# Kernel tuning notes

Hardware: AMD Instinct MI355X
Metric: run time of the kernel (lower is better)

## Reference

```python
import jax, jax.numpy as jnp
import numpy as np

N_NODES = 50000
N_EDGES = 800000
NEG_SLOPE = 0.2  # GATConv default
BN_EPS = 1e-5


def _seg_softmax(logits, seg, n):
    # per-target-node softmax over incoming edges (PyG softmax w/ +1e-16)
    m = jax.ops.segment_max(logits, seg, num_segments=n)
    m = jnp.where(jnp.isfinite(m), m, 0.0)
    e = jnp.exp(logits - m[seg])
    s = jax.ops.segment_sum(e, seg, num_segments=n)
    return e / (s[seg] + 1e-16)


def _gat_conv(x, src, dst, W, a_src, a_dst, b, concat):
    # x: [N, Fin]; W: [Fin, H*C]; a_src/a_dst: [H, C]
    n = x.shape[0]
    H, C = a_src.shape
    h = (x @ W).reshape(n, H, C)
    al_s = jnp.einsum('nhc,hc->nh', h, a_src)
    al_d = jnp.einsum('nhc,hc->nh', h, a_dst)
    logits = jax.nn.leaky_relu(al_s[src] + al_d[dst], NEG_SLOPE)  # [E, H]
    alpha = _seg_softmax(logits, dst, n)                           # [E, H]
    out = jax.ops.segment_sum(h[src] * alpha[:, :, None], dst, num_segments=n)
    out = out.reshape(n, H * C) if concat else out.mean(axis=1)
    return out + b


def _bn(x, g, b):
    mu = jnp.mean(x, axis=0)
    var = jnp.mean((x - mu) ** 2, axis=0)
    return (x - mu) * jax.lax.rsqrt(var + BN_EPS) * g + b


def _gat_params(key, fin, heads, ch, scale=0.1):
    k1, k2, k3 = jax.random.split(key, 3)
    W = jax.random.normal(k1, (fin, heads * ch), jnp.float32) * scale
    a_s = jax.random.normal(k2, (heads, ch), jnp.float32) * scale
    a_d = jax.random.normal(k3, (heads, ch), jnp.float32) * scale
    return W, a_s, a_d


def setup_inputs() -> dict:
    key = jax.random.key(0)
    ks = jax.random.split(key, 12)
    inp = {}
    inp['x'] = jax.random.normal(ks[0], (N_NODES, 3), jnp.float32)
    inp['edge_index'] = jax.random.randint(ks[1], (2, N_EDGES), 0, N_NODES, jnp.int64 if jax.config.jax_enable_x64 else jnp.int32)
    inp['W11'], inp['as11'], inp['ad11'] = _gat_params(ks[2], 3, 8, 8)
    inp['b11'] = jnp.zeros((64,), jnp.float32)
    inp['W12'], inp['as12'], inp['ad12'] = _gat_params(ks[3], 64, 8, 8)
    inp['b12'] = jnp.zeros((64,), jnp.float32)
    inp['g1'] = jnp.ones((64,), jnp.float32)
    inp['be1'] = jnp.zeros((64,), jnp.float32)
    inp['W21'], inp['as21'], inp['ad21'] = _gat_params(ks[4], 64, 8, 32)
    inp['b21'] = jnp.zeros((256,), jnp.float32)
    inp['W22'], inp['as22'], inp['ad22'] = _gat_params(ks[5], 256, 8, 32)
    inp['b22'] = jnp.zeros((256,), jnp.float32)
    inp['g2'] = jnp.ones((256,), jnp.float32)
    inp['be2'] = jnp.zeros((256,), jnp.float32)
    inp['W31'], inp['as31'], inp['ad31'] = _gat_params(ks[6], 256, 8, 64)
    inp['b31'] = jnp.zeros((512,), jnp.float32)
    inp['W32'], inp['as32'], inp['ad32'] = _gat_params(ks[7], 512, 8, 1)
    inp['b32'] = jnp.zeros((1,), jnp.float32)
    return inp


def reference(x, edge_index,
              W11, as11, ad11, b11, W12, as12, ad12, b12, g1, be1,
              W21, as21, ad21, b21, W22, as22, ad22, b22, g2, be2,
              W31, as31, ad31, b31, W32, as32, ad32, b32):
    n = x.shape[0]
    loops = jnp.arange(n, dtype=edge_index.dtype)
    src = jnp.concatenate([edge_index[0], loops])  # add_self_loops=True
    dst = jnp.concatenate([edge_index[1], loops])
    # GAT(3, 64, 2): conv -> relu -> conv
    h = jax.nn.relu(_gat_conv(x, src, dst, W11, as11, ad11, b11, True))
    h = _gat_conv(h, src, dst, W12, as12, ad12, b12, True)
    h = jax.nn.leaky_relu(_bn(h, g1, be1), 0.1)
    # GAT(64, 256, 2)
    h = jax.nn.relu(_gat_conv(h, src, dst, W21, as21, ad21, b21, True))
    h = _gat_conv(h, src, dst, W22, as22, ad22, b22, True)
    h = jax.nn.leaky_relu(_bn(h, g2, be2), 0.1)
    # GAT(256, 512, 2, 1): conv -> relu -> conv(concat=False)
    h = jax.nn.relu(_gat_conv(h, src, dst, W31, as31, ad31, b31, True))
    h = _gat_conv(h, src, dst, W32, as32, ad32, b32, False)
    return jax.nn.sigmoid(h)
```

## Files before the change

### kernel.cpp

```cpp
#include <hip/hip_runtime.h>
#include <math.h>

typedef short short8 __attribute__((ext_vector_type(8)));
typedef short short4v __attribute__((ext_vector_type(4)));
typedef float f32x4 __attribute__((ext_vector_type(4)));

__device__ __forceinline__ unsigned short f2bf(float v){
  unsigned u = __builtin_bit_cast(unsigned, v);
  u += 0x7FFFu + ((u >> 16) & 1u);
  return (unsigned short)(u >> 16);
}
__device__ __forceinline__ float bf2f(unsigned short b){
  unsigned u = ((unsigned)b) << 16;
  return __builtin_bit_cast(float, u);
}

__global__ void k_deg(const int* __restrict__ dstv, int* __restrict__ deg, int E){
  int e = blockIdx.x*blockDim.x + threadIdx.x;
  if (e < E) atomicAdd(&deg[dstv[e]], 1);
}

__global__ void k_scan(const int* __restrict__ deg, int* __restrict__ off,
                       int* __restrict__ cursor, int N){
  __shared__ int sh[1024];
  __shared__ int carry_s;
  int t = threadIdx.x;
  if (t == 0) carry_s = 0;
  __syncthreads();
  for (int base = 0; base < N; base += 1024){
    int i = base + t;
    int v = (i < N) ? deg[i] : 0;
    sh[t] = v;
    __syncthreads();
    for (int d = 1; d < 1024; d <<= 1){
      int tmp = (t >= d) ? sh[t-d] : 0;
      __syncthreads();
      sh[t] += tmp;
      __syncthreads();
    }
    int inc = sh[t];
    int c = carry_s;
    if (i < N){ off[i+1] = c + inc; cursor[i] = c + inc - v; }
    __syncthreads();
    if (t == 1023) carry_s = c + sh[1023];
    __syncthreads();
  }
  if (t == 0) off[0] = 0;
}

__global__ void k_fill(const int* __restrict__ srcv, const int* __restrict__ dstv,
                       int* __restrict__ cursor, int* __restrict__ csr, int E){
  int e = blockIdx.x*blockDim.x + threadIdx.x;
  if (e < E){
    int d = dstv[e];
    int p = atomicAdd(&cursor[d], 1);
    csr[p] = srcv[e];
  }
}

__global__ void k_prepB(const float* __restrict__ W, unsigned short* __restrict__ bh,
                        unsigned short* __restrict__ bl, int K, int kpshift, int Nn){
  int Kp = 1 << kpshift;
  int i = blockIdx.x*blockDim.x + threadIdx.x;
  if (i >= Nn*Kp) return;
  int n = i >> kpshift, k = i & (Kp-1);
  float v = (k < K) ? W[(size_t)k*Nn + n] : 0.0f;
  unsigned short h = f2bf(v);
  bh[i] = h;
  bl[i] = f2bf(v - bf2f(h));
}

template<int BN>
__global__ __launch_bounds__((BN==64)?256:512)
void gemm_mfma(const float* __restrict__ A, const unsigned short* __restrict__ Bh,
               const unsigned short* __restrict__ Bl,
               const float* __restrict__ a_s, const float* __restrict__ a_d,
               unsigned short* __restrict__ Pb, float* __restrict__ D, int M, int K){
  constexpr int WAVES   = (BN==64) ? 4 : 8;
  constexpr int BLOCK   = WAVES*64;
  constexpr int WAVES_N = BN/64;
  constexpr int WAVES_M = WAVES/WAVES_N;
  constexpr int WM      = 64/WAVES_M;
  constexpr int MF      = WM/16;
  constexpr int CH      = (BN==512)?64 : (BN==256)?32 : 8;
  const int Kp = (K + 63) & ~(int)63;

  __shared__ char lds[16384];

  int tid  = threadIdx.x;
  int lane = tid & 63;
  int wid  = tid >> 6;
  int wn = wid % WAVES_N;
  int wm = wid / WAVES_N;
  int n0w = wn*64;
  int wm0 = wm*WM;
  int m0 = blockIdx.x * 64;

  f32x4 acc[MF][4];
  #pragma unroll
  for (int i = 0; i < MF; ++i)
    #pragma unroll
    for (int j = 0; j < 4; ++j)
      acc[i][j] = (f32x4){0.f,0.f,0.f,0.f};

  constexpr int SITER = 512/BLOCK;

  for (int k0 = 0; k0 < Kp; k0 += 64){
    __syncthreads();
    #pragma unroll
    for (int it = 0; it < SITER; ++it){
      int i = it*BLOCK + tid;
      int row = i >> 3, c8 = i & 7;
      int gm = m0 + row;
      int gk = k0 + c8*8;
      float v[8];
      if (gm < M && gk + 8 <= K){
        const float* ap = A + (size_t)gm*K + gk;
        float4 x0 = *(const float4*)ap;
        float4 x1 = *(const float4*)(ap+4);
        v[0]=x0.x; v[1]=x0.y; v[2]=x0.z; v[3]=x0.w;
        v[4]=x1.x; v[5]=x1.y; v[6]=x1.z; v[7]=x1.w;
      } else {
        #pragma unroll
        for (int j=0;j<8;++j){
          int gkj = gk + j;
          v[j] = (gm < M && gkj < K) ? A[(size_t)gm*K + gkj] : 0.0f;
        }
      }
      short8 hi, lo;
      #pragma unroll
      for (int j=0;j<8;++j){
        unsigned short hb = f2bf(v[j]);
        hi[j] = (short)hb;
        lo[j] = (short)f2bf(v[j] - bf2f(hb));
      }
      int off = row*128 + ((c8 ^ (row&7))<<4);
      *(short8*)(lds + off) = hi;
      *(short8*)(lds + 8192 + off) = lo;
    }
    __syncthreads();
    #pragma unroll
    for (int kk = 0; kk < 2; ++kk){
      short8 bhf[4], blf[4];
      #pragma unroll
      for (int nf = 0; nf < 4; ++nf){
        int ncol = n0w + nf*16 + (lane & 15);
        int kidx = k0 + kk*32 + ((lane>>4)<<3);
        size_t bo = (size_t)ncol*Kp + kidx;
        bhf[nf] = *(const short8*)(Bh + bo);
        blf[nf] = *(const short8*)(Bl + bo);
      }
      #pragma unroll
      for (int mt = 0; mt < MF; ++mt){
        int row = wm0 + mt*16 + (lane & 15);
        int c8 = kk*4 + (lane>>4);
        int off = row*128 + ((c8 ^ (row&7))<<4);
        short8 ah = *(const short8*)(lds + off);
        short8 al = *(const short8*)(lds + 8192 + off);
        #pragma unroll
        for (int nf = 0; nf < 4; ++nf){
          acc[mt][nf] = __builtin_amdgcn_mfma_f32_16x16x32_bf16(ah, bhf[nf], acc[mt][nf], 0,0,0);
          acc[mt][nf] = __builtin_amdgcn_mfma_f32_16x16x32_bf16(ah, blf[nf], acc[mt][nf], 0,0,0);
          acc[mt][nf] = __builtin_amdgcn_mfma_f32_16x16x32_bf16(al, bhf[nf], acc[mt][nf], 0,0,0);
        }
      }
    }
  }

  float asv[4], adv[4];
  #pragma unroll
  for (int nf=0; nf<4; ++nf){
    int gcol = n0w + nf*16 + (lane&15);
    asv[nf] = a_s[gcol];
    adv[nf] = a_d[gcol];
  }
  #pragma unroll
  for (int mt = 0; mt < MF; ++mt){
    #pragma unroll
    for (int r = 0; r < 4; ++r){
      int gm = m0 + wm0 + mt*16 + ((lane>>4)<<2) + r;
      bool ok = gm < M;
      #pragma unroll
      for (int nf=0;nf<4;++nf){
        if (ok) Pb[(size_t)gm*BN + n0w + nf*16 + (lane&15)] = f2bf(acc[mt][nf][r]);
      }
      float* dp = D + (size_t)gm*16;
      if constexpr (CH == 64){
        float ps = acc[mt][0][r]*asv[0] + acc[mt][1][r]*asv[1]
                 + acc[mt][2][r]*asv[2] + acc[mt][3][r]*asv[3];
        float pd = acc[mt][0][r]*adv[0] + acc[mt][1][r]*adv[1]
                 + acc[mt][2][r]*adv[2] + acc[mt][3][r]*adv[3];
        #pragma unroll
        for (int d2=1; d2<16; d2<<=1){ ps += __shfl_xor(ps,d2,64); pd += __shfl_xor(pd,d2,64); }
        if (ok && (lane&15)==0){
          int head = n0w >> 6;
          dp[head] = ps;
          dp[8 + head] = pd;
        }
      } else if constexpr (CH == 32){
        float ps0 = acc[mt][0][r]*asv[0] + acc[mt][1][r]*asv[1];
        float ps1 = acc[mt][2][r]*asv[2] + acc[mt][3][r]*asv[3];
        float pd0 = acc[mt][0][r]*adv[0] + acc[mt][1][r]*adv[1];
        float pd1 = acc[mt][2][r]*adv[2] + acc[mt][3][r]*adv[3];
        #pragma unroll
        for (int d2=1; d2<16; d2<<=1){
          ps0 += __shfl_xor(ps0,d2,64); ps1 += __shfl_xor(ps1,d2,64);
          pd0 += __shfl_xor(pd0,d2,64); pd1 += __shfl_xor(pd1,d2,64);
        }
        if (ok && (lane&15)==0){
          int head = n0w >> 5;
          dp[head]     = ps0;
          dp[head + 1] = ps1;
          dp[8 + head]     = pd0;
          dp[8 + head + 1] = pd1;
        }
      } else {
        #pragma unroll
        for (int nf=0;nf<4;++nf){
          float ps = acc[mt][nf][r]*asv[nf];
          float pd = acc[mt][nf][r]*adv[nf];
          #pragma unroll
          for (int d2=1; d2<8; d2<<=1){ ps += __shfl_xor(ps,d2,64); pd += __shfl_xor(pd,d2,64); }
          if (ok && (lane&7)==0){
            int head = nf*2 + ((lane>>3)&1);
            dp[head]     = ps;
            dp[8 + head] = pd;
          }
        }
      }
    }
  }
}

__global__ __launch_bounds__(256)
void gemm_f32(const float* __restrict__ A, const float* __restrict__ B,
              float* __restrict__ C, int M, int K, int Nn){
  __shared__ float As[16][65];
  __shared__ float Bs[16][64];
  int tid = threadIdx.x;
  int tx = tid & 15, ty = tid >> 4;
  int m0 = blockIdx.x * 64, n0 = blockIdx.y * 64;
  float acc[4][4] = {};
  for (int k0 = 0; k0 < K; k0 += 16){
    #pragma unroll
    for (int it = 0; it < 4; ++it){
      int idx = it*256 + tid;
      int mm = idx >> 4, kk = idx & 15;
      int gm = m0 + mm, gk = k0 + kk;
      As[kk][mm] = (gm < M && gk < K) ? A[(size_t)gm*K + gk] : 0.0f;
    }
    #pragma unroll
    for (int it = 0; it < 4; ++it){
      int idx = it*256 + tid;
      int kk = idx >> 6, nn = idx & 63;
      int gk = k0 + kk, gn = n0 + nn;
      Bs[kk][nn] = (gk < K && gn < Nn) ? B[(size_t)gk*Nn + gn] : 0.0f;
    }
    __syncthreads();
    #pragma unroll
    for (int kk = 0; kk < 16; ++kk){
      float a[4], b[4];
      #pragma unroll
      for (int i = 0; i < 4; ++i) a[i] = As[kk][ty*4+i];
      #pragma unroll
      for (int j = 0; j < 4; ++j) b[j] = Bs[kk][tx*4+j];
      #pragma unroll
      for (int i = 0; i < 4; ++i)
        #pragma unroll
        for (int j = 0; j < 4; ++j)
          acc[i][j] += a[i]*b[j];
    }
    __syncthreads();
  }
  #pragma unroll
  for (int i = 0; i < 4; ++i){
    int gm = m0 + ty*4 + i;
    if (gm >= M) continue;
    int gn = n0 + tx*4;
    #pragma unroll
    for (int j = 0; j < 4; ++j)
      if (gn + j < Nn) C[(size_t)gm*Nn + gn + j] = acc[i][j];
  }
}

__global__ void k_attn8(const float* __restrict__ ht, const float* __restrict__ a_s,
                        const float* __restrict__ a_d, float* __restrict__ als,
                        float* __restrict__ ald, int N){
  int i = blockIdx.x*blockDim.x + threadIdx.x;
  if (i >= N*8) return;
  int h = i & 7;
  float v = ht[i];
  als[i] = v * a_s[h];
  ald[i] = v * a_d[h];
}

template<int HC, int ACT>
__global__ __launch_bounds__(256)
void k_agg(const unsigned short* __restrict__ Pb, const float* __restrict__ D,
           const int* __restrict__ off, const int* __restrict__ csr,
           const float* __restrict__ bias, float* __restrict__ outb, int N){
  constexpr int R = HC/64;
  __shared__ float salpha[4][512];
  int lane = threadIdx.x & 63;
  int wid  = threadIdx.x >> 6;
  int n = blockIdx.x*4 + wid;
  if (n >= N) return;
  int o0 = off[n], deg = off[n+1]-o0;
  int myh = lane >> 3;

  float aldn[8];
  {
    const float* dn = D + (size_t)n*16 + 8;
    float4 x0 = *(const float4*)dn;
    float4 x1 = *(const float4*)(dn+4);
    aldn[0]=x0.x; aldn[1]=x0.y; aldn[2]=x0.z; aldn[3]=x0.w;
    aldn[4]=x1.x; aldn[5]=x1.y; aldn[6]=x1.z; aldn[7]=x1.w;
  }

  float acc[R];
  #pragma unroll
  for (int j=0;j<R;++j) acc[j]=0.f;

  if (deg < 64){
    int nE = deg + 1;
    int myidx = (lane < deg) ? csr[o0+lane] : n;
    bool active = (lane < nE);
    float v[8];
    {
      const float* dp = D + (size_t)myidx*16;
      float4 x0 = *(const float4*)dp;
      float4 x1 = *(const float4*)(dp+4);
      float t[8] = {x0.x,x0.y,x0.z,x0.w,x1.x,x1.y,x1.z,x1.w};
      #pragma unroll
      for (int h=0;h<8;++h){
        float u = t[h] + aldn[h];
        u = u > 0.f ? u : 0.2f*u;
        v[h] = active ? u : -1e30f;
      }
    }
    float m[8];
    #pragma unroll
    for (int h=0;h<8;++h) m[h]=v[h];
    #pragma unroll
    for (int d=1; d<64; d<<=1)
      #pragma unroll
      for (int h=0;h<8;++h) m[h] = fmaxf(m[h], __shfl_xor(m[h], d, 64));
    float sv[8], s[8];
    #pragma unroll
    for (int h=0;h<8;++h){ sv[h] = active ? __expf(v[h]-m[h]) : 0.f; s[h]=sv[h]; }
    #pragma unroll
    for (int d=1; d<64; d<<=1)
      #pragma unroll
      for (int h=0;h<8;++h) s[h] += __shfl_xor(s[h], d, 64);
    if (active){
      #pragma unroll
      for (int h=0;h<8;++h) salpha[wid][lane*8+h] = sv[h] / (s[h] + 1e-16f);
    }
    asm volatile("s_waitcnt lgkmcnt(0)" ::: "memory");

    for (int e=0; e<nE; ++e){
      int src = __shfl(myidx, e, 64);
      float alpha = salpha[wid][e*8 + myh];
      const unsigned short* hp = Pb + (size_t)src*HC + lane*R;
      if constexpr (R == 1){
        acc[0] += alpha * bf2f(hp[0]);
      } else if constexpr (R == 4){
        short4v w = *(const short4v*)hp;
        #pragma unroll
        for (int j=0;j<4;++j) acc[j] += alpha * bf2f((unsigned short)w[j]);
      } else {
        short8 w = *(const short8*)hp;
        #pragma unroll
        for (int j=0;j<8;++j) acc[j] += alpha * bf2f((unsigned short)w[j]);
      }
    }
  } else {
    float m[8];
    #pragma unroll
    for (int h=0;h<8;++h) m[h] = -1e30f;
    for (int e = lane; e <= deg; e += 64){
      int src = (e < deg) ? csr[o0+e] : n;
      const float* ap = D + (size_t)src*16;
      #pragma unroll
      for (int h=0;h<8;++h){
        float u = ap[h] + aldn[h];
        u = u > 0.f ? u : 0.2f*u;
        m[h] = fmaxf(m[h], u);
      }
    }
    #pragma unroll
    for (int d=1; d<64; d<<=1)
      #pragma unroll
      for (int h=0;h<8;++h) m[h] = fmaxf(m[h], __shfl_xor(m[h], d, 64));
    float s[8] = {0,0,0,0,0,0,0,0};
    for (int e = lane; e <= deg; e += 64){
      int src = (e < deg) ? csr[o0+e] : n;
      const float* ap = D + (size_t)src*16;
      #pragma unroll
      for (int h=0;h<8;++h){
        float u = ap[h] + aldn[h];
        u = u > 0.f ? u : 0.2f*u;
        s[h] += __expf(u - m[h]);
      }
    }
    #pragma unroll
    for (int d=1; d<64; d<<=1)
      #pragma unroll
      for (int h=0;h<8;++h) s[h] += __shfl_xor(s[h], d, 64);
    float mh = m[myh];
    float rsh = 1.0f/(s[myh] + 1e-16f);
    float adh = aldn[myh];
    for (int e = 0; e <= deg; ++e){
      int src = (e < deg) ? csr[o0+e] : n;
      float u = D[(size_t)src*16 + myh] + adh;
      u = u > 0.f ? u : 0.2f*u;
      float alpha = __expf(u - mh) * rsh;
      const unsigned short* hp = Pb + (size_t)src*HC + lane*R;
      if constexpr (R == 1){
        acc[0] += alpha * bf2f(hp[0]);
      } else if constexpr (R == 4){
        short4v w = *(const short4v*)hp;
        #pragma unroll
        for (int j=0;j<4;++j) acc[j] += alpha * bf2f((unsigned short)w[j]);
      } else {
        short8 w = *(const short8*)hp;
        #pragma unroll
        for (int j=0;j<8;++j) acc[j] += alpha * bf2f((unsigned short)w[j]);
      }
    }
  }

  #pragma unroll
  for (int j = 0; j < R; ++j){
    int f = lane*R + j;
    float v = acc[j] + bias[f];
    if (ACT == 1) v = fmaxf(v, 0.0f);
    outb[(size_t)n*HC + f] = v;
  }
}

__global__ void k_bn_stats(const float* __restrict__ x, float* __restrict__ gsum,
                           float* __restrict__ gsq, int N, int HC){
  int f = threadIdx.x;
  float s = 0.f, q = 0.f;
  for (int r = blockIdx.x; r < N; r += gridDim.x){
    float v = x[(size_t)r*HC + f];
    s += v; q += v*v;
  }
  atomicAdd(&gsum[f], s);
  atomicAdd(&gsq[f], q);
}

__global__ void k_bn_apply(float* __restrict__ x, const float* __restrict__ gsum,
                           const float* __restrict__ gsq, const float* __restrict__ g,
                           const float* __restrict__ b, int N, int HC){
  int i = blockIdx.x*blockDim.x + threadIdx.x;
  int total = N*HC;
  if (i >= total) return;
  int f = i % HC;
  float inv = 1.0f/(float)N;
  float mu  = gsum[f]*inv;
  float var = gsq[f]*inv - mu*mu;
  float v = (x[i]-mu)*rsqrtf(var+1e-5f)*g[f] + b[f];
  x[i] = v > 0.f ? v : 0.1f*v;
}

__global__ void k_final(const float* __restrict__ ht8, const float* __restrict__ als,
                        const float* __restrict__ ald, const int* __restrict__ off,
                        const int* __restrict__ csr, const float* __restrict__ b32,
                        float* __restrict__ outp, int N){
  int n = blockIdx.x*blockDim.x + threadIdx.x;
  if (n >= N) return;
  int o0 = off[n], deg = off[n+1]-o0;
  float aldn[8], m[8], s[8], agg[8];
  #pragma unroll
  for (int h = 0; h < 8; ++h){ aldn[h] = ald[n*8+h]; m[h] = -1e30f; s[h]=0.f; agg[h]=0.f; }
  for (int e = 0; e <= deg; ++e){
    int src = (e < deg) ? csr[o0+e] : n;
    #pragma unroll
    for (int h = 0; h < 8; ++h){
      float v = als[(size_t)src*8+h] + aldn[h];
      v = v > 0.f ? v : 0.2f*v;
      m[h] = fmaxf(m[h], v);
    }
  }
  for (int e = 0; e <= deg; ++e){
    int src = (e < deg) ? csr[o0+e] : n;
    #pragma unroll
    for (int h = 0; h < 8; ++h){
      float v = als[(size_t)src*8+h] + aldn[h];
      v = v > 0.f ? v : 0.2f*v;
      float ex = __expf(v - m[h]);
      s[h] += ex;
      agg[h] += ex * ht8[(size_t)src*8+h];
    }
  }
  float o = 0.f;
  #pragma unroll
  for (int h = 0; h < 8; ++h) o += agg[h]/(s[h]+1e-16f);
  o = o*0.125f + b32[0];
  outp[n] = 1.0f/(1.0f + __expf(-o));
}

extern "C" void kernel_launch(void* const* d_in, const int* in_sizes, int n_in,
                              void* d_out, int out_size, void* d_ws, size_t ws_size,
                              hipStream_t stream){
  int N = in_sizes[0]/3;
  int E = in_sizes[1]/2;
  const float* x    = (const float*)d_in[0];
  const int*   ei   = (const int*)  d_in[1];
  const float* W11  = (const float*)d_in[2];
  const float* as11 = (const float*)d_in[3];
  const float* ad11 = (const float*)d_in[4];
  const float* b11  = (const float*)d_in[5];
  const float* W12  = (const float*)d_in[6];
  const float* as12 = (const float*)d_in[7];
  const float* ad12 = (const float*)d_in[8];
  const float* b12  = (const float*)d_in[9];
  const float* g1   = (const float*)d_in[10];
  const float* be1  = (const float*)d_in[11];
  const float* W21  = (const float*)d_in[12];
  const float* as21 = (const float*)d_in[13];
  const float* ad21 = (const float*)d_in[14];
  const float* b21  = (const float*)d_in[15];
  const float* W22  = (const float*)d_in[16];
  const float* as22 = (const float*)d_in[17];
  const float* ad22 = (const float*)d_in[18];
  const float* b22  = (const float*)d_in[19];
  const float* g2   = (const float*)d_in[20];
  const float* be2  = (const float*)d_in[21];
  const float* W31  = (const float*)d_in[22];
  const float* as31 = (const float*)d_in[23];
  const float* ad31 = (const float*)d_in[24];
  const float* b31  = (const float*)d_in[25];
  const float* W32  = (const float*)d_in[26];
  const float* as32 = (const float*)d_in[27];
  const float* ad32 = (const float*)d_in[28];
  const float* b32  = (const float*)d_in[29];

  char* ws = (char*)d_ws;
  size_t o = 0;
  auto alloc = [&](size_t bytes)->char*{
    char* p = ws + o;
    o = (o + bytes + 255) & ~(size_t)255;
    return p;
  };
  int*   deg    = (int*)  alloc((size_t)N*4);
  int*   off    = (int*)  alloc((size_t)(N+1)*4);
  int*   cursor = (int*)  alloc((size_t)N*4);
  int*   csr    = (int*)  alloc((size_t)E*4);
  unsigned short* bth = (unsigned short*)alloc(131072*2);
  unsigned short* btl = (unsigned short*)alloc(131072*2);
  float* als8   = (float*)alloc((size_t)N*8*4);
  float* ald8   = (float*)alloc((size_t)N*8*4);
  float* h8     = (float*)alloc((size_t)N*8*4);
  float* bsum   = (float*)alloc(256*4);
  float* bsq    = (float*)alloc(256*4);
  unsigned short* Pb = (unsigned short*)alloc((size_t)N*512*2);
  float* D      = (float*)alloc((size_t)N*16*4);
  float* Q      = (float*)alloc((size_t)N*512*4);
  (void)ws_size;

  hipMemsetAsync(deg, 0, (size_t)N*4, stream);
  int eb = (E+255)/256;
  k_deg <<<eb, 256, 0, stream>>>(ei+E, deg, E);
  k_scan<<<1, 1024, 0, stream>>>(deg, off, cursor, N);
  k_fill<<<eb, 256, 0, stream>>>(ei, ei+E, cursor, csr, E);

  int mb = (N+63)/64;
  int nb4 = (N+3)/4;

  k_prepB<<<(64*64)/256, 256, 0, stream>>>(W11, bth, btl, 3, 6, 64);
  gemm_mfma<64><<<mb, 256, 0, stream>>>(x, bth, btl, as11, ad11, Pb, D, N, 3);
  k_agg<64,1><<<nb4, 256, 0, stream>>>(Pb, D, off, csr, b11, Q, N);

  k_prepB<<<(64*64)/256, 256, 0, stream>>>(W12, bth, btl, 64, 6, 64);
  gemm_mfma<64><<<mb, 256, 0, stream>>>(Q, bth, btl, as12, ad12, Pb, D, N, 64);
  k_agg<64,0><<<nb4, 256, 0, stream>>>(Pb, D, off, csr, b12, Q, N);
  hipMemsetAsync(bsum, 0, 64*4, stream);
  hipMemsetAsync(bsq,  0, 64*4, stream);
  k_bn_stats<<<512, 64, 0, stream>>>(Q, bsum, bsq, N, 64);
  k_bn_apply<<<(N*64+255)/256, 256, 0, stream>>>(Q, bsum, bsq, g1, be1, N, 64);

  k_prepB<<<(256*64)/256, 256, 0, stream>>>(W21, bth, btl, 64, 6, 256);
  gemm_mfma<256><<<mb, 512, 0, stream>>>(Q, bth, btl, as21, ad21, Pb, D, N, 64);
  k_agg<256,1><<<nb4, 256, 0, stream>>>(Pb, D, off, csr, b21, Q, N);

  k_prepB<<<(256*256)/256, 256, 0, stream>>>(W22, bth, btl, 256, 8, 256);
  gemm_mfma<256><<<mb, 512, 0, stream>>>(Q, bth, btl, as22, ad22, Pb, D, N, 256);
  k_agg<256,0><<<nb4, 256, 0, stream>>>(Pb, D, off, csr, b22, Q, N);
  hipMemsetAsync(bsum, 0, 256*4, stream);
  hipMemsetAsync(bsq,  0, 256*4, stream);
  k_bn_stats<<<512, 256, 0, stream>>>(Q, bsum, bsq, N, 256);
  k_bn_apply<<<(N*256+255)/256, 256, 0, stream>>>(Q, bsum, bsq, g2, be2, N, 256);

  k_prepB<<<(512*256)/256, 256, 0, stream>>>(W31, bth, btl, 256, 8, 512);
  gemm_mfma<512><<<mb, 512, 0, stream>>>(Q, bth, btl, as31, ad31, Pb, D, N, 256);
  k_agg<512,1><<<nb4, 256, 0, stream>>>(Pb, D, off, csr, b31, Q, N);

  {
    dim3 g((N+63)/64, 1);
    gemm_f32<<<g, 256, 0, stream>>>(Q, W32, h8, N, 512, 8);
  }
  k_attn8<<<(N*8+255)/256, 256, 0, stream>>>(h8, as32, ad32, als8, ald8, N);
  k_final<<<(N+255)/256, 256, 0, stream>>>(h8, als8, ald8, off, csr, b32,
                                           (float*)d_out, N);
}
```

Before: 1.251 ms.

## Fuse BN into GEMM loads, wave-parallel final layer, shuffle-based scan

Several independent changes land together. The BatchNorm apply pass is replaced by a tiny coefficient kernel, and the scale/shift plus leaky-ReLU are folded into the GEMM's A-tile load, removing a full read/write pass over the activations. The last aggregation writes bf16, and a new wave-per-row dot-product kernel replaces the tiled fp32 GEMM for the 512->8 projection. The final softmax-aggregate kernel now uses one wave per node with shuffle reductions instead of one thread per node. The degree scan also switches to wave shuffles. Rounding the 512-wide input of the last projection to bf16 adds precision loss.

Result: faster. 1.146 ms (-8.4%).

```diff
diff --git a/kernel.cpp b/kernel.cpp
--- a/kernel.cpp
+++ b/kernel.cpp
@@ -22,30 +22,44 @@
 
 __global__ void k_scan(const int* __restrict__ deg, int* __restrict__ off,
                        int* __restrict__ cursor, int N){
-  __shared__ int sh[1024];
-  __shared__ int carry_s;
-  int t = threadIdx.x;
-  if (t == 0) carry_s = 0;
+  __shared__ int wpre[16];
+  __shared__ int s_tot;
+  __shared__ int carry;
+  int tid = threadIdx.x;
+  int lane = tid & 63, wv = tid >> 6;
+  if (tid == 0) carry = 0;
   __syncthreads();
   for (int base = 0; base < N; base += 1024){
-    int i = base + t;
+    int i = base + tid;
     int v = (i < N) ? deg[i] : 0;
-    sh[t] = v;
+    int incl = v;
+    #pragma unroll
+    for (int d = 1; d < 64; d <<= 1){
+      int t = __shfl_up(incl, d, 64);
+      if (lane >= d) incl += t;
+    }
+    if (lane == 63) wpre[wv] = incl;
     __syncthreads();
-    for (int d = 1; d < 1024; d <<= 1){
-      int tmp = (t >= d) ? sh[t-d] : 0;
-      __syncthreads();
-      sh[t] += tmp;
-      __syncthreads();
-    }
-    int inc = sh[t];
-    int c = carry_s;
-    if (i < N){ off[i+1] = c + inc; cursor[i] = c + inc - v; }
+    if (tid < 16){
+      int x = wpre[tid];
+      int ix = x;
+      #pragma unroll
+      for (int d = 1; d < 16; d <<= 1){
+        int t = __shfl_up(ix, d, 16);
+        if (tid >= d) ix += t;
+      }
+      wpre[tid] = ix - x;
+      if (tid == 15) s_tot = ix;
+    }
     __syncthreads();
-    if (t == 1023) carry_s = c + sh[1023];
+    int c = carry;
+    int excl = c + wpre[wv] + (incl - v);
+    if (i < N){ off[i+1] = excl + v; cursor[i] = excl; }
     __syncthreads();
-  }
-  if (t == 0) off[0] = 0;
+    if (tid == 0) carry = c + s_tot;
+    __syncthreads();
+  }
+  if (tid == 0) off[0] = 0;
 }
 
 __global__ void k_fill(const int* __restrict__ srcv, const int* __restrict__ dstv,
@@ -70,10 +84,24 @@
   bl[i] = f2bf(v - bf2f(h));
 }
 
-template<int BN>
+__global__ void k_bn_coef(const float* __restrict__ bsum, const float* __restrict__ bsq,
+                          const float* __restrict__ g, const float* __restrict__ b,
+                          float* __restrict__ sc, float* __restrict__ sh,
+                          float invN, int HC){
+  int f = threadIdx.x + blockIdx.x*blockDim.x;
+  if (f >= HC) return;
+  float mu  = bsum[f]*invN;
+  float var = bsq[f]*invN - mu*mu;
+  float rs  = rsqrtf(var + 1e-5f) * g[f];
+  sc[f] = rs;
+  sh[f] = b[f] - mu*rs;
+}
+
+template<int BN, int MODE>
 __global__ __launch_bounds__((BN==64)?256:512)
 void gemm_mfma(const float* __restrict__ A, const unsigned short* __restrict__ Bh,
                const unsigned short* __restrict__ Bl,
+               const float* __restrict__ bnsc, const float* __restrict__ bnsh,
                const float* __restrict__ a_s, const float* __restrict__ a_d,
                unsigned short* __restrict__ Pb, float* __restrict__ D, int M, int K){
   constexpr int WAVES   = (BN==64) ? 4 : 8;
@@ -120,11 +148,26 @@
         float4 x1 = *(const float4*)(ap+4);
         v[0]=x0.x; v[1]=x0.y; v[2]=x0.z; v[3]=x0.w;
         v[4]=x1.x; v[5]=x1.y; v[6]=x1.z; v[7]=x1.w;
+        if constexpr (MODE == 1){
+          #pragma unroll
+          for (int j=0;j<8;++j){
+            float u = v[j]*bnsc[gk+j] + bnsh[gk+j];
+            v[j] = u > 0.f ? u : 0.1f*u;
+          }
+        }
       } else {
         #pragma unroll
         for (int j=0;j<8;++j){
           int gkj = gk + j;
-          v[j] = (gm < M && gkj < K) ? A[(size_t)gm*K + gkj] : 0.0f;
+          bool ok = (gm < M && gkj < K);
+          float u = ok ? A[(size_t)gm*K + gkj] : 0.0f;
+          if constexpr (MODE == 1){
+            if (ok){
+              u = u*bnsc[gkj] + bnsh[gkj];
+              u = u > 0.f ? u : 0.1f*u;
+            }
+          }
+          v[j] = u;
         }
       }
       short8 hi, lo;
@@ -232,73 +275,11 @@
   }
 }
 
-__global__ __launch_bounds__(256)
-void gemm_f32(const float* __restrict__ A, const float* __restrict__ B,
-              float* __restrict__ C, int M, int K, int Nn){
-  __shared__ float As[16][65];
-  __shared__ float Bs[16][64];
-  int tid = threadIdx.x;
-  int tx = tid & 15, ty = tid >> 4;
-  int m0 = blockIdx.x * 64, n0 = blockIdx.y * 64;
-  float acc[4][4] = {};
-  for (int k0 = 0; k0 < K; k0 += 16){
-    #pragma unroll
-    for (int it = 0; it < 4; ++it){
-      int idx = it*256 + tid;
-      int mm = idx >> 4, kk = idx & 15;
-      int gm = m0 + mm, gk = k0 + kk;
-      As[kk][mm] = (gm < M && gk < K) ? A[(size_t)gm*K + gk] : 0.0f;
-    }
-    #pragma unroll
-    for (int it = 0; it < 4; ++it){
-      int idx = it*256 + tid;
-      int kk = idx >> 6, nn = idx & 63;
-      int gk = k0 + kk, gn = n0 + nn;
-      Bs[kk][nn] = (gk < K && gn < Nn) ? B[(size_t)gk*Nn + gn] : 0.0f;
-    }
-    __syncthreads();
-    #pragma unroll
-    for (int kk = 0; kk < 16; ++kk){
-      float a[4], b[4];
-      #pragma unroll
-      for (int i = 0; i < 4; ++i) a[i] = As[kk][ty*4+i];
-      #pragma unroll
-      for (int j = 0; j < 4; ++j) b[j] = Bs[kk][tx*4+j];
-      #pragma unroll
-      for (int i = 0; i < 4; ++i)
-        #pragma unroll
-        for (int j = 0; j < 4; ++j)
-          acc[i][j] += a[i]*b[j];
-    }
-    __syncthreads();
-  }
-  #pragma unroll
-  for (int i = 0; i < 4; ++i){
-    int gm = m0 + ty*4 + i;
-    if (gm >= M) continue;
-    int gn = n0 + tx*4;
-    #pragma unroll
-    for (int j = 0; j < 4; ++j)
-      if (gn + j < Nn) C[(size_t)gm*Nn + gn + j] = acc[i][j];
-  }
-}
-
-__global__ void k_attn8(const float* __restrict__ ht, const float* __restrict__ a_s,
-                        const float* __restrict__ a_d, float* __restrict__ als,
-                        float* __restrict__ ald, int N){
-  int i = blockIdx.x*blockDim.x + threadIdx.x;
-  if (i >= N*8) return;
-  int h = i & 7;
-  float v = ht[i];
-  als[i] = v * a_s[h];
-  ald[i] = v * a_d[h];
-}
-
-template<int HC, int ACT>
+template<int HC, int ACT, int OBF>
 __global__ __launch_bounds__(256)
 void k_agg(const unsigned short* __restrict__ Pb, const float* __restrict__ D,
            const int* __restrict__ off, const int* __restrict__ csr,
-           const float* __restrict__ bias, float* __restrict__ outb, int N){
+           const float* __restrict__ bias, void* __restrict__ outv, int N){
   constexpr int R = HC/64;
   __shared__ float salpha[4][512];
   int lane = threadIdx.x & 63;
@@ -435,7 +416,10 @@
     int f = lane*R + j;
     float v = acc[j] + bias[f];
     if (ACT == 1) v = fmaxf(v, 0.0f);
-    outb[(size_t)n*HC + f] = v;
+    if constexpr (OBF == 1)
+      ((unsigned short*)outv)[(size_t)n*HC + f] = f2bf(v);
+    else
+      ((float*)outv)[(size_t)n*HC + f] = v;
   }
 }
 
@@ -451,55 +435,142 @@
   atomicAdd(&gsq[f], q);
 }
 
-__global__ void k_bn_apply(float* __restrict__ x, const float* __restrict__ gsum,
-                           const float* __restrict__ gsq, const float* __restrict__ g,
-                           const float* __restrict__ b, int N, int HC){
-  int i = blockIdx.x*blockDim.x + threadIdx.x;
-  int total = N*HC;
-  if (i >= total) return;
-  int f = i % HC;
-  float inv = 1.0f/(float)N;
-  float mu  = gsum[f]*inv;
-  float var = gsq[f]*inv - mu*mu;
-  float v = (x[i]-mu)*rsqrtf(var+1e-5f)*g[f] + b[f];
-  x[i] = v > 0.f ? v : 0.1f*v;
-}
-
-__global__ void k_final(const float* __restrict__ ht8, const float* __restrict__ als,
-                        const float* __restrict__ ald, const int* __restrict__ off,
-                        const int* __restrict__ csr, const float* __restrict__ b32,
-                        float* __restrict__ outp, int N){
-  int n = blockIdx.x*blockDim.x + threadIdx.x;
+__global__ __launch_bounds__(256)
+void gemm8(const unsigned short* __restrict__ Qb, const float* __restrict__ W,
+           float* __restrict__ h8, int M){
+  int lane = threadIdx.x & 63;
+  int gw = (blockIdx.x*blockDim.x + threadIdx.x) >> 6;
+  int nw = (gridDim.x*blockDim.x) >> 6;
+  float w[8][8];
+  const float* wp = W + lane*64;
+  #pragma unroll
+  for (int j=0;j<8;++j){
+    float4 a = *(const float4*)(wp + j*8);
+    float4 b = *(const float4*)(wp + j*8 + 4);
+    w[j][0]=a.x; w[j][1]=a.y; w[j][2]=a.z; w[j][3]=a.w;
+    w[j][4]=b.x; w[j][5]=b.y; w[j][6]=b.z; w[j][7]=b.w;
+  }
+  for (int n = gw; n < M; n += nw){
+    short8 v8 = *(const short8*)(Qb + (size_t)n*512 + lane*8);
+    float p[8] = {0,0,0,0,0,0,0,0};
+    #pragma unroll
+    for (int j=0;j<8;++j){
+      float x = bf2f((unsigned short)v8[j]);
+      #pragma unroll
+      for (int o=0;o<8;++o) p[o] += x * w[j][o];
+    }
+    #pragma unroll
+    for (int d=1; d<64; d<<=1)
+      #pragma unroll
+      for (int o=0;o<8;++o) p[o] += __shfl_xor(p[o], d, 64);
+    if (lane == 0){
+      float4 y0 = make_float4(p[0],p[1],p[2],p[3]);
+      float4 y1 = make_float4(p[4],p[5],p[6],p[7]);
+      *(float4*)(h8 + (size_t)n*8)     = y0;
+      *(float4*)(h8 + (size_t)n*8 + 4) = y1;
+    }
+  }
+}
+
+__global__ __launch_bounds__(256)
+void k_final(const float* __restrict__ h8, const float* __restrict__ a_s,
+             const float* __restrict__ a_d, const int* __restrict__ off,
+             const int* __restrict__ csr, const float* __restrict__ b32,
+             float* __restrict__ outp, int N){
+  int lane = threadIdx.x & 63;
+  int wv   = threadIdx.x >> 6;
+  int n = blockIdx.x*4 + wv;
   if (n >= N) return;
   int o0 = off[n], deg = off[n+1]-o0;
-  float aldn[8], m[8], s[8], agg[8];
+  float asv[8], adv[8];
   #pragma unroll
-  for (int h = 0; h < 8; ++h){ aldn[h] = ald[n*8+h]; m[h] = -1e30f; s[h]=0.f; agg[h]=0.f; }
-  for (int e = 0; e <= deg; ++e){
-    int src = (e < deg) ? csr[o0+e] : n;
-    #pragma unroll
-    for (int h = 0; h < 8; ++h){
-      float v = als[(size_t)src*8+h] + aldn[h];
-      v = v > 0.f ? v : 0.2f*v;
-      m[h] = fmaxf(m[h], v);
-    }
-  }
-  for (int e = 0; e <= deg; ++e){
-    int src = (e < deg) ? csr[o0+e] : n;
-    #pragma unroll
-    for (int h = 0; h < 8; ++h){
-      float v = als[(size_t)src*8+h] + aldn[h];
-      v = v > 0.f ? v : 0.2f*v;
-      float ex = __expf(v - m[h]);
-      s[h] += ex;
-      agg[h] += ex * ht8[(size_t)src*8+h];
-    }
-  }
-  float o = 0.f;
-  #pragma unroll
-  for (int h = 0; h < 8; ++h) o += agg[h]/(s[h]+1e-16f);
-  o = o*0.125f + b32[0];
-  outp[n] = 1.0f/(1.0f + __expf(-o));
+  for (int h=0;h<8;++h){ asv[h]=a_s[h]; adv[h]=a_d[h]; }
+  float aldn[8];
+  {
+    const float* hp = h8 + (size_t)n*8;
+    float4 x0 = *(const float4*)hp;
+    float4 x1 = *(const float4*)(hp+4);
+    float hn[8] = {x0.x,x0.y,x0.z,x0.w,x1.x,x1.y,x1.z,x1.w};
+    #pragma unroll
+    for (int h=0;h<8;++h) aldn[h] = hn[h]*adv[h];
+  }
+
+  if (deg < 64){
+    int nE = deg + 1;
+    int src = (lane < deg) ? csr[o0+lane] : n;
+    bool act = (lane < nE);
+    float hs[8];
+    {
+      const float* hp = h8 + (size_t)src*8;
+      float4 x0 = *(const float4*)hp;
+      float4 x1 = *(const float4*)(hp+4);
+      hs[0]=x0.x; hs[1]=x0.y; hs[2]=x0.z; hs[3]=x0.w;
+      hs[4]=x1.x; hs[5]=x1.y; hs[6]=x1.z; hs[7]=x1.w;
+    }
+    float v[8];
+    #pragma unroll
+    for (int h=0;h<8;++h){
+      float u = hs[h]*asv[h] + aldn[h];
+      u = u > 0.f ? u : 0.2f*u;
+      v[h] = act ? u : -1e30f;
+    }
+    float m[8];
+    #pragma unroll
+    for (int h=0;h<8;++h) m[h]=v[h];
+    #pragma unroll
+    for (int d=1; d<64; d<<=1)
+      #pragma unroll
+      for (int h=0;h<8;++h) m[h] = fmaxf(m[h], __shfl_xor(m[h], d, 64));
+    float s[8], t[8];
+    #pragma unroll
+    for (int h=0;h<8;++h){
+      float e = act ? __expf(v[h]-m[h]) : 0.f;
+      s[h]=e; t[h]=e*hs[h];
+    }
+    #pragma unroll
+    for (int d=1; d<64; d<<=1)
+      #pragma unroll
+      for (int h=0;h<8;++h){
+        s[h] += __shfl_xor(s[h], d, 64);
+        t[h] += __shfl_xor(t[h], d, 64);
+      }
+    if (lane == 0){
+      float o = 0.f;
+      #pragma unroll
+      for (int h=0;h<8;++h) o += t[h]/(s[h]+1e-16f);
+      o = o*0.125f + b32[0];
+      outp[n] = 1.0f/(1.0f + __expf(-o));
+    }
+  } else if (lane == 0){
+    float m[8], s[8], agg[8];
+    #pragma unroll
+    for (int h=0;h<8;++h){ m[h]=-1e30f; s[h]=0.f; agg[h]=0.f; }
+    for (int e = 0; e <= deg; ++e){
+      int src = (e < deg) ? csr[o0+e] : n;
+      #pragma unroll
+      for (int h=0;h<8;++h){
+        float u = h8[(size_t)src*8+h]*asv[h] + aldn[h];
+        u = u > 0.f ? u : 0.2f*u;
+        m[h] = fmaxf(m[h], u);
+      }
+    }
+    for (int e = 0; e <= deg; ++e){
+      int src = (e < deg) ? csr[o0+e] : n;
+      #pragma unroll
+      for (int h=0;h<8;++h){
+        float u = h8[(size_t)src*8+h]*asv[h] + aldn[h];
+        u = u > 0.f ? u : 0.2f*u;
+        float ex = __expf(u - m[h]);
+        s[h] += ex;
+        agg[h] += ex * h8[(size_t)src*8+h];
+      }
+    }
+    float o = 0.f;
+    #pragma unroll
+    for (int h=0;h<8;++h) o += agg[h]/(s[h]+1e-16f);
+    o = o*0.125f + b32[0];
+    outp[n] = 1.0f/(1.0f + __expf(-o));
+  }
 }
 
 extern "C" void kernel_launch(void* const* d_in, const int* in_sizes, int n_in,
@@ -551,14 +622,15 @@
   int*   csr    = (int*)  alloc((size_t)E*4);
   unsigned short* bth = (unsigned short*)alloc(131072*2);
   unsigned short* btl = (unsigned short*)alloc(131072*2);
-  float* als8   = (float*)alloc((size_t)N*8*4);
-  float* ald8   = (float*)alloc((size_t)N*8*4);
   float* h8     = (float*)alloc((size_t)N*8*4);
-  float* bsum   = (float*)alloc(256*4);
-  float* bsq    = (float*)alloc(256*4);
+  float* bsum   = (float*)alloc(1024);
+  float* bsq    = (float*)alloc(1024);
+  float* bnsc   = (float*)alloc(1024);
+  float* bnsh   = (float*)alloc(1024);
   unsigned short* Pb = (unsigned short*)alloc((size_t)N*512*2);
   float* D      = (float*)alloc((size_t)N*16*4);
   float* Q      = (float*)alloc((size_t)N*512*4);
+  unsigned short* Qb = (unsigned short*)alloc((size_t)N*512*2);
   (void)ws_size;
 
   hipMemsetAsync(deg, 0, (size_t)N*4, stream);
@@ -569,40 +641,40 @@
 
   int mb = (N+63)/64;
   int nb4 = (N+3)/4;
+  float invN = 1.0f/(float)N;
 
   k_prepB<<<(64*64)/256, 256, 0, stream>>>(W11, bth, btl, 3, 6, 64);
-  gemm_mfma<64><<<mb, 256, 0, stream>>>(x, bth, btl, as11, ad11, Pb, D, N, 3);
-  k_agg<64,1><<<nb4, 256, 0, stream>>>(Pb, D, off, csr, b11, Q, N);
+  gemm_mfma<64,0><<<mb, 256, 0, stream>>>(x, bth, btl, nullptr, nullptr,
+                                          as11, ad11, Pb, D, N, 3);
+  k_agg<64,1,0><<<nb4, 256, 0, stream>>>(Pb, D, off, csr, b11, Q, N);
 
   k_prepB<<<(64*64)/256, 256, 0, stream>>>(W12, bth, btl, 64, 6, 64);
-  gemm_mfma<64><<<mb, 256, 0, stream>>>(Q, bth, btl, as12, ad12, Pb, D, N, 64);
-  k_agg<64,0><<<nb4, 256, 0, stream>>>(Pb, D, off, csr, b12, Q, N);
-  hipMemsetAsync(bsum, 0, 64*4, stream);
-  hipMemsetAsync(bsq,  0, 64*4, stream);
+  gemm_mfma<64,0><<<mb, 256, 0, stream>>>(Q, bth, btl, nullptr, nullptr,
+                                          as12, ad12, Pb, D, N, 64);
+  k_agg<64,0,0><<<nb4, 256, 0, stream>>>(Pb, D, off, csr, b12, Q, N);
+  hipMemsetAsync(bsum, 0, 2048, stream);
   k_bn_stats<<<512, 64, 0, stream>>>(Q, bsum, bsq, N, 64);
-  k_bn_apply<<<(N*64+255)/256, 256, 0, stream>>>(Q, bsum, bsq, g1, be1, N, 64);
+  k_bn_coef<<<1, 64, 0, stream>>>(bsum, bsq, g1, be1, bnsc, bnsh, invN, 64);
 
   k_prepB<<<(256*64)/256, 256, 0, stream>>>(W21, bth, btl, 64, 6, 256);
-  gemm_mfma<256><<<mb, 512, 0, stream>>>(Q, bth, btl, as21, ad21, Pb, D, N, 64);
-  k_agg<256,1><<<nb4, 256, 0, stream>>>(Pb, D, off, csr, b21, Q, N);
+  gemm_mfma<256,1><<<mb, 512, 0, stream>>>(Q, bth, btl, bnsc, bnsh,
+                                           as21, ad21, Pb, D, N, 64);
+  k_agg<256,1,0><<<nb4, 256, 0, stream>>>(Pb, D, off, csr, b21, Q, N);
 
   k_prepB<<<(256*256)/256, 256, 0, stream>>>(W22, bth, btl, 256, 8, 256);
-  gemm_mfma<256><<<mb, 512, 0, stream>>>(Q, bth, btl, as22, ad22, Pb, D, N, 256);
-  k_agg<256,0><<<nb4, 256, 0, stream>>>(Pb, D, off, csr, b22, Q, N);
-  hipMemsetAsync(bsum, 0, 256*4, stream);
-  hipMemsetAsync(bsq,  0, 256*4, stream);
+  gemm_mfma<256,0><<<mb, 512, 0, stream>>>(Q, bth, btl, nullptr, nullptr,
+                                           as22, ad22, Pb, D, N, 256);
+  k_agg<256,0,0><<<nb4, 256, 0, stream>>>(Pb, D, off, csr, b22, Q, N);
+  hipMemsetAsync(bsum, 0, 2048, stream);
   k_bn_stats<<<512, 256, 0, stream>>>(Q, bsum, bsq, N, 256);
-  k_bn_apply<<<(N*256+255)/256, 256, 0, stream>>>(Q, bsum, bsq, g2, be2, N, 256);
+  k_bn_coef<<<1, 256, 0, stream>>>(bsum, bsq, g2, be2, bnsc, bnsh, invN, 256);
 
   k_prepB<<<(512*256)/256, 256, 0, stream>>>(W31, bth, btl, 256, 8, 512);
-  gemm_mfma<512><<<mb, 512, 0, stream>>>(Q, bth, btl, as31, ad31, Pb, D, N, 256);
-  k_agg<512,1><<<nb4, 256, 0, stream>>>(Pb, D, off, csr, b31, Q, N);
-
-  {
-    dim3 g((N+63)/64, 1);
-    gemm_f32<<<g, 256, 0, stream>>>(Q, W32, h8, N, 512, 8);
-  }
-  k_attn8<<<(N*8+255)/256, 256, 0, stream>>>(h8, as32, ad32, als8, ald8, N);
-  k_final<<<(N+255)/256, 256, 0, stream>>>(h8, als8, ald8, off, csr, b32,
-                                           (float*)d_out, N);
-}
+  gemm_mfma<512,1><<<mb, 512, 0, stream>>>(Q, bth, btl, bnsc, bnsh,
+                                           as31, ad31, Pb, D, N, 256);
+  k_agg<512,1,1><<<nb4, 256, 0, stream>>>(Pb, D, off, csr, b31, Qb, N);
+
+  gemm8<<<1024, 256, 0, stream>>>(Qb, W32, h8, N);
+  k_final<<<nb4, 256, 0, stream>>>(h8, as32, ad32, off, csr, b32,
+                                   (float*)d_out, N);
+}
```
